# Kernel optimization log

Measured on AMD Instinct MI355X. Metric: run time of the kernel, lower is better.

Reference implementation:

```python
import jax, jax.numpy as jnp
import numpy as np

B, C, Himg, Wimg = 4, 256, 64, 64
HID = 256
K = 8
EPS_NORM = 1e-12
BN_EPS = 1e-5


def setup_inputs() -> dict:
    key = jax.random.key(0)
    ks = jax.random.split(key, 14)
    s = lambda fan: 1.0 / np.sqrt(fan)
    inp = {
        "features": jax.random.normal(ks[0], (B, C, Himg, Wimg), dtype=jnp.float32),
        # HypergraphConv 0: theta (C->HID), phi (HID->HID). Weights stored [in,out].
        "theta0_w": jax.random.normal(ks[1], (C, HID), dtype=jnp.float32) * s(C),
        "theta0_b": jnp.zeros((HID,), jnp.float32),
        "phi0_w": jax.random.normal(ks[2], (HID, HID), dtype=jnp.float32) * s(HID),
        "phi0_b": jnp.zeros((HID,), jnp.float32),
        # HypergraphConv 1: theta (HID->HID), phi (HID->HID)
        "theta1_w": jax.random.normal(ks[3], (HID, HID), dtype=jnp.float32) * s(HID),
        "theta1_b": jnp.zeros((HID,), jnp.float32),
        "phi1_w": jax.random.normal(ks[4], (HID, HID), dtype=jnp.float32) * s(HID),
        "phi1_b": jnp.zeros((HID,), jnp.float32),
        # out_proj: 1x1 conv HID->C, stored as [HID, C]
        "proj_w": jax.random.normal(ks[5], (HID, C), dtype=jnp.float32) * s(HID),
        "proj_b": jnp.zeros((C,), jnp.float32),
        # BatchNorm2d affine params
        "bn_gamma": jnp.ones((C,), jnp.float32),
        "bn_beta": jnp.zeros((C,), jnp.float32),
    }
    return inp


def _build_hypergraph(features):
    # features: [B, C, H, W] -> nodes [B, N, C]; incidence from batch 0 only
    b, c, h, w = features.shape
    n = h * w
    feat_flat = features.reshape(b, c, n).transpose(0, 2, 1)  # [B, N, C]
    f0 = feat_flat[0]  # [N, C] (original computes full-batch similarity but uses [0])
    f0n = f0 / jnp.maximum(jnp.linalg.norm(f0, axis=-1, keepdims=True), EPS_NORM)
    sim = f0n @ f0n.T  # [N, N]
    _, idx = jax.lax.top_k(sim, K)  # [N, K]
    rows = idx.reshape(-1)
    cols = jnp.repeat(jnp.arange(n), K)
    Hm = jnp.zeros((n, n), jnp.float32).at[rows, cols].set(1.0)  # [N, E=N]
    # L1 column normalization (F.normalize p=1 dim=0)
    Hn = Hm / jnp.maximum(Hm.sum(axis=0, keepdims=True), EPS_NORM)
    return Hn, feat_flat


def _hconv(x, Hn, tw, tb, pw, pb):
    # x: [B, N, Cin]
    xt = x @ tw + tb  # [B, N, Cout]
    ef = jnp.einsum('ne,bnc->bec', Hn, xt)  # H^T @ x_theta -> edge feats
    xp = ef @ pw + pb  # [B, E, Cout]
    return jnp.einsum('ne,bec->bnc', Hn, xp)  # H @ x_phi


def reference(features, theta0_w, theta0_b, phi0_w, phi0_b,
              theta1_w, theta1_b, phi1_w, phi1_b,
              proj_w, proj_b, bn_gamma, bn_beta):
    b, c, h, w = features.shape
    Hn, x = _build_hypergraph(features)
    x = jax.nn.relu(_hconv(x, Hn, theta0_w, theta0_b, phi0_w, phi0_b))
    x = jax.nn.relu(_hconv(x, Hn, theta1_w, theta1_b, phi1_w, phi1_b)) + x
    # back to [B, HID, H, W] then 1x1 conv
    x = x.transpose(0, 2, 1).reshape(b, HID, h, w)
    x = jnp.einsum('bihw,io->bohw', x, proj_w) + proj_b[None, :, None, None]
    # BatchNorm2d (training mode: batch statistics, biased variance)
    mean = x.mean(axis=(0, 2, 3))
    var = x.var(axis=(0, 2, 3))
    xn = (x - mean[None, :, None, None]) * jax.lax.rsqrt(var + BN_EPS)[None, :, None, None]
    xn = xn * bn_gamma[None, :, None, None] + bn_beta[None, :, None, None]
    return features + xn
```

## Files before the change

### kernel.cpp

```cpp
#include <hip/hip_runtime.h>

namespace {

constexpr int NB = 4;
constexpr int NC = 256;
constexpr int NN = 4096;

typedef __attribute__((ext_vector_type(8))) short bf8;
typedef __attribute__((ext_vector_type(4))) float f4;
typedef unsigned short ushort_t;
typedef unsigned long long ull;

__device__ __forceinline__ float bf2f(unsigned short u) {
  return __uint_as_float(((unsigned)u) << 16);
}
__device__ __forceinline__ unsigned short f2bf(float f) {
  unsigned x = __float_as_uint(f);
  return (unsigned short)((x + 0x7FFFu + ((x >> 16) & 1u)) >> 16);
}
__device__ __forceinline__ unsigned enc_f(float f) {
  unsigned u = __float_as_uint(f);
  return (u & 0x80000000u) ? ~u : (u | 0x80000000u);
}

__device__ __forceinline__ void insd(double* b, double k) {
  b[7] = fmax(b[7], k);
#pragma unroll
  for (int p = 7; p >= 1; --p) {
    double hi = fmax(b[p-1], b[p]);
    double lo = fmin(b[p-1], b[p]);
    b[p-1] = hi; b[p] = lo;
  }
}

__device__ __forceinline__ double shfl_xor_d(double v, int m) {
  ull u = __double_as_longlong(v);
  unsigned lo = (unsigned)(u & 0xFFFFFFFFull), hi = (unsigned)(u >> 32);
  lo = (unsigned)__shfl_xor((int)lo, m);
  hi = (unsigned)__shfl_xor((int)hi, m);
  return __longlong_as_double(((ull)hi << 32) | (ull)lo);
}

template<int MAXS>
__device__ __forceinline__ void shfl_merged(double* b) {
#pragma unroll
  for (int s = 1; s <= MAXS; s <<= 1) {
    double tmp[8];
#pragma unroll
    for (int k = 0; k < 8; ++k) tmp[k] = shfl_xor_d(b[k], s);
#pragma unroll
    for (int k = 0; k < 8; ++k) insd(b, tmp[k]);
  }
}

__global__ __launch_bounds__(256) void norm_kernel(const float* __restrict__ feat,
                                                   float* __restrict__ inv,
                                                   int* __restrict__ counts,
                                                   float* __restrict__ bnsum) {
  int n = blockIdx.x * 256 + threadIdx.x;
  counts[n] = 0;
  if (n < 2 * NC) bnsum[n] = 0.f;
  float ss = 0.f;
  for (int c = 0; c < NC; ++c) { float v = feat[(size_t)c * NN + n]; ss = fmaf(v, v, ss); }
  inv[n] = 1.f / fmaxf(sqrtf(ss), 1e-12f);
}

__global__ __launch_bounds__(256) void feat2bf_kernel(const float* __restrict__ feat,
                                                      const float* __restrict__ inv,
                                                      unsigned short* __restrict__ xin,
                                                      unsigned short* __restrict__ Xhi,
                                                      unsigned short* __restrict__ Xlo) {
  __shared__ float tile[64][65];
  int n0 = blockIdx.x * 64, c0 = blockIdx.y * 64, b = blockIdx.z;
  int tid = threadIdx.x;
#pragma unroll
  for (int i = 0; i < 4; ++i) {
    int u = tid + i * 256; int cr = u >> 4, q = u & 15;
    float4 v = *(const float4*)&feat[((size_t)b * NC + c0 + cr) * NN + n0 + q * 4];
    tile[cr][q*4+0] = v.x; tile[cr][q*4+1] = v.y; tile[cr][q*4+2] = v.z; tile[cr][q*4+3] = v.w;
  }
  __syncthreads();
#pragma unroll
  for (int i = 0; i < 4; ++i) {
    int u = tid + i * 256; int nr = u >> 4, q = u & 15;
    float x0 = tile[q*4+0][nr], x1 = tile[q*4+1][nr];
    float x2 = tile[q*4+2][nr], x3 = tile[q*4+3][nr];
    ushort4 o;
    o.x = f2bf(x0); o.y = f2bf(x1); o.z = f2bf(x2); o.w = f2bf(x3);
    *(ushort4*)&xin[((size_t)(b << 12) + n0 + nr) * NC + c0 + q * 4] = o;
    if (b == 0) {
      float iv = inv[n0 + nr];
      float y0 = x0 * iv, y1 = x1 * iv, y2 = x2 * iv, y3 = x3 * iv;
      ushort4 h, l;
      h.x = f2bf(y0); l.x = f2bf(y0 - bf2f(h.x));
      h.y = f2bf(y1); l.y = f2bf(y1 - bf2f(h.y));
      h.z = f2bf(y2); l.z = f2bf(y2 - bf2f(h.z));
      h.w = f2bf(y3); l.w = f2bf(y3 - bf2f(h.w));
      size_t oo = (size_t)(n0 + nr) * NC + c0 + q * 4;
      *(ushort4*)&Xhi[oo] = h;
      *(ushort4*)&Xlo[oo] = l;
    }
  }
}

__global__ __launch_bounds__(256) void wcvt_kernel(const float* __restrict__ w0,
                                                   const float* __restrict__ w1,
                                                   const float* __restrict__ w2,
                                                   const float* __restrict__ w3,
                                                   const float* __restrict__ w4,
                                                   unsigned short* __restrict__ Wt) {
  __shared__ float tile[64][65];
  int z = blockIdx.z;
  const float* W = (z == 0) ? w0 : (z == 1) ? w1 : (z == 2) ? w2 : (z == 3) ? w3 : w4;
  int k0 = blockIdx.x * 64, n0 = blockIdx.y * 64;
  int tid = threadIdx.x;
#pragma unroll
  for (int i = 0; i < 4; ++i) {
    int u = tid + i * 256; int kr = u >> 4, q = u & 15;
    float4 v = *(const float4*)&W[(size_t)(k0 + kr) * NC + n0 + q * 4];
    tile[kr][q*4+0] = v.x; tile[kr][q*4+1] = v.y; tile[kr][q*4+2] = v.z; tile[kr][q*4+3] = v.w;
  }
  __syncthreads();
#pragma unroll
  for (int i = 0; i < 4; ++i) {
    int u = tid + i * 256; int nr = u >> 4, q = u & 15;
    ushort4 o;
    o.x = f2bf(tile[q*4+0][nr]); o.y = f2bf(tile[q*4+1][nr]);
    o.z = f2bf(tile[q*4+2][nr]); o.w = f2bf(tile[q*4+3][nr]);
    *(ushort4*)&Wt[(size_t)z * 65536 + (size_t)(n0 + nr) * NC + k0 + q * 4] = o;
  }
}

__global__ __launch_bounds__(512, 6) void simtop_kernel(const unsigned short* __restrict__ Xhi,
                                                        const unsigned short* __restrict__ Xlo,
                                                        double* __restrict__ cand) {
  __shared__ __align__(16) char lds[40960];
  float (*simT)[132] = (float(*)[132])(lds);

  int tid = threadIdx.x, wave = tid >> 6, lane = tid & 63;
  int wm = wave >> 2, wn = wave & 3;
  int orig = blockIdx.x;
  int bid = (orig & 7) * 66 + (orig >> 3);
  int pi = (int)((sqrtf(8.f * (float)bid + 1.f) - 1.f) * 0.5f);
  while ((pi + 1) * (pi + 2) / 2 <= bid) ++pi;
  while (pi * (pi + 1) / 2 > bid) --pi;
  int pj = bid - pi * (pi + 1) / 2;
  int m0 = pj * 128, n0 = pi * 128;

  int sr = tid >> 2;
  int q  = tid & 3;
  int qp = q ^ (sr & 3);
  const ushort_t* gAh = Xhi + (size_t)(m0 + sr) * NC + q * 8;
  const ushort_t* gAl = Xlo + (size_t)(m0 + sr) * NC + q * 8;
  const ushort_t* gBh = Xhi + (size_t)(n0 + sr) * NC + q * 8;
  const ushort_t* gBl = Xlo + (size_t)(n0 + sr) * NC + q * 8;
  int dst = sr * 80 + qp * 16;

  f4 acc[4][2];
#pragma unroll
  for (int i = 0; i < 4; ++i)
#pragma unroll
    for (int j = 0; j < 2; ++j) acc[i][j] = (f4){0.f, 0.f, 0.f, 0.f};

#pragma unroll
  for (int kk = 0; kk < 8; ++kk) {
    uint4 a0 = *(const uint4*)(gAh + kk * 32);
    uint4 a1 = *(const uint4*)(gAl + kk * 32);
    uint4 b0 = *(const uint4*)(gBh + kk * 32);
    uint4 b1 = *(const uint4*)(gBl + kk * 32);
    *(uint4*)(lds +     0 + dst) = a0;
    *(uint4*)(lds + 10240 + dst) = a1;
    *(uint4*)(lds + 20480 + dst) = b0;
    *(uint4*)(lds + 30720 + dst) = b1;
    __syncthreads();
    {
      int qr = lane >> 4;
      bf8 ah[4], al[4], bh[2], bl[2];
#pragma unroll
      for (int mf = 0; mf < 4; ++mf) {
        int rr = wm*64 + mf*16 + (lane & 15);
        int off = rr * 80 + ((qr ^ (rr & 3)) * 16);
        ah[mf] = *(const bf8*)(lds +     0 + off);
        al[mf] = *(const bf8*)(lds + 10240 + off);
      }
#pragma unroll
      for (int nf = 0; nf < 2; ++nf) {
        int rr = wn*32 + nf*16 + (lane & 15);
        int off = rr * 80 + ((qr ^ (rr & 3)) * 16);
        bh[nf] = *(const bf8*)(lds + 20480 + off);
        bl[nf] = *(const bf8*)(lds + 30720 + off);
      }
#pragma unroll
      for (int nf = 0; nf < 2; ++nf)
#pragma unroll
        for (int mf = 0; mf < 4; ++mf) {
          acc[mf][nf] = __builtin_amdgcn_mfma_f32_16x16x32_bf16(ah[mf], bh[nf], acc[mf][nf], 0, 0, 0);
          acc[mf][nf] = __builtin_amdgcn_mfma_f32_16x16x32_bf16(ah[mf], bl[nf], acc[mf][nf], 0, 0, 0);
          acc[mf][nf] = __builtin_amdgcn_mfma_f32_16x16x32_bf16(al[mf], bh[nf], acc[mf][nf], 0, 0, 0);
        }
    }
    __syncthreads();
  }

  double c8[8];
  int ccol = 0, cseg = 0;
  bool docol = (pi != pj) && (tid >= 256);
  if (docol) {
    ccol = (tid - 256) >> 1; cseg = tid & 1;
#pragma unroll
    for (int k = 0; k < 8; ++k) c8[k] = 0.0;
  }

#pragma unroll
  for (int h = 0; h < 2; ++h) {
    if (h) __syncthreads();
    if (wm == h) {
#pragma unroll
      for (int mf = 0; mf < 4; ++mf)
#pragma unroll
        for (int nf = 0; nf < 2; ++nf) {
          int cl = wn*32 + nf*16 + (lane & 15);
          int rb = mf*16 + (lane >> 4)*4;
#pragma unroll
          for (int r = 0; r < 4; ++r) simT[rb + r][cl] = acc[mf][nf][r];
        }
    }
    __syncthreads();
    if (tid < 256) {
      int rl = tid >> 2, q4 = tid & 3;
      const float* rowp = &simT[rl][q4 * 32];
      double b8[8] = {0,0,0,0,0,0,0,0};
#pragma unroll
      for (int i = 0; i < 8; ++i) {
        int off = ((i + q4 * 2) & 7) * 4;
        float4 v = *(const float4*)(rowp + off);
        unsigned jb = 0xFFFu - (unsigned)(n0 + q4 * 32 + off);
        insd(b8, (double)((((ull)enc_f(v.x)) << 12) | (ull)(jb    )));
        insd(b8, (double)((((ull)enc_f(v.y)) << 12) | (ull)(jb - 1)));
        insd(b8, (double)((((ull)enc_f(v.z)) << 12) | (ull)(jb - 2)));
        insd(b8, (double)((((ull)enc_f(v.w)) << 12) | (ull)(jb - 3)));
      }
      shfl_merged<2>(b8);
      if (q4 == 0) {
        double* dp = cand + (size_t)(m0 + h * 64 + rl) * 256 + pi * 8;
#pragma unroll
        for (int k = 0; k < 8; ++k) dp[k] = b8[k];
      }
    } else if (docol) {
#pragma unroll
      for (int i = 0; i < 32; ++i) {
        int ir = (i + cseg * 7) & 31;
        int rloc = cseg * 32 + ir;
        float v = simT[rloc][ccol];
        unsigned jb = 0xFFFu - (unsigned)(m0 + h * 64 + rloc);
        insd(c8, (double)((((ull)enc_f(v)) << 12) | (ull)jb));
      }
    }
  }
  if (docol) {
    shfl_merged<1>(c8);
    if (cseg == 0) {
      double* dp = cand + (size_t)(n0 + ccol) * 256 + pj * 8;
#pragma unroll
      for (int k = 0; k < 8; ++k) dp[k] = c8[k];
    }
  }
}

__global__ __launch_bounds__(256) void merge_kernel(const double* __restrict__ cand,
                                                    int* __restrict__ idx8,
                                                    int* __restrict__ counts) {
  int t = blockIdx.x * 256 + threadIdx.x;
  int row = t >> 3, part = t & 7;
  const double* cp = cand + (size_t)row * 256 + part * 32;
  double b8[8] = {0,0,0,0,0,0,0,0};
  for (int g = 0; g < 4; ++g) {
#pragma unroll 1
    for (int k = 0; k < 8; ++k) {
      double key = cp[g * 8 + k];
      if (key <= b8[7]) break;
      insd(b8, key);
    }
  }
  shfl_merged<4>(b8);
  if (part == 0) {
#pragma unroll
    for (int k = 0; k < 8; ++k) {
      ull K = (ull)b8[k];
      int j = 0xFFF - (int)(K & 0xFFFull);
      idx8[row * 8 + k] = j;
      atomicAdd(&counts[j], 1);
    }
  }
}

__global__ __launch_bounds__(256) void scan_kernel(const int* __restrict__ counts,
                                                   int* __restrict__ offsets,
                                                   int* __restrict__ cursor) {
  __shared__ int ssum[256];
  __shared__ int sbase[257];
  int t = threadIdx.x;
  int loc[16];
  int s = 0;
#pragma unroll
  for (int i = 0; i < 16; ++i) { loc[i] = s; s += counts[t*16 + i]; }
  ssum[t] = s;
  __syncthreads();
  if (t == 0) {
    int acc = 0;
    for (int i = 0; i < 256; ++i) { sbase[i] = acc; acc += ssum[i]; }
    sbase[256] = acc;
  }
  __syncthreads();
  int b0 = sbase[t];
#pragma unroll
  for (int i = 0; i < 16; ++i) {
    int off = b0 + loc[i];
    offsets[t*16 + i] = off;
    cursor [t*16 + i] = off;
  }
  if (t == 0) offsets[NN] = sbase[256];
}

__global__ __launch_bounds__(256) void fill_kernel(const int* __restrict__ idx8,
                                                   int* __restrict__ cursor,
                                                   int* __restrict__ edgelist) {
  int t = blockIdx.x * 256 + threadIdx.x;
  int n = idx8[t];
  int pos = atomicAdd(&cursor[n], 1);
  edgelist[pos] = t >> 3;
}

template<int OUTF32, int BNS, int GATHER>
__global__ __launch_bounds__(512) void gemm_bf16_kernel(const unsigned short* __restrict__ A,
                                                        const unsigned short* __restrict__ Wt,
                                                        const float* __restrict__ bias,
                                                        void* __restrict__ outp,
                                                        float* __restrict__ bnsum,
                                                        const int* __restrict__ idx8) {
  __shared__ ushort_t sA[128][72];
  __shared__ ushort_t sB[128][72];
  __shared__ int sIdx[128][8];
  int tid = threadIdx.x, wave = tid >> 6, lane = tid & 63;
  int wm = wave >> 2, wn = wave & 3;
  int n0 = blockIdx.x * 128, m0 = blockIdx.y * 128;
  size_t bbase = 0;
  if constexpr (GATHER) {
    int e0 = m0 & 4095;
    bbase = ((size_t)(m0 >> 12) << 12) * NC;
#pragma unroll
    for (int u = tid; u < 1024; u += 512) ((int*)sIdx)[u] = idx8[e0 * 8 + u];
    __syncthreads();
  }
  f4 acc[4][2];
#pragma unroll
  for (int i = 0; i < 4; ++i)
#pragma unroll
    for (int j = 0; j < 2; ++j) acc[i][j] = (f4){0.f, 0.f, 0.f, 0.f};

  for (int k0 = 0; k0 < NC; k0 += 64) {
#pragma unroll
    for (int i = 0; i < 2; ++i) {
      int u = tid + i * 512; int r = u >> 3; int qq = u & 7;
      int qp = (qq ^ ((r >> 1) & 7)) * 8;
      if constexpr (GATHER) {
        float s[8] = {0.f,0.f,0.f,0.f,0.f,0.f,0.f,0.f};
#pragma unroll
        for (int k = 0; k < 8; ++k) {
          int nn = sIdx[r][k];
          uint4 v = *(const uint4*)&A[bbase + (size_t)nn * NC + k0 + qq * 8];
          s[0] += bf2f((unsigned short)(v.x & 0xFFFF)); s[1] += bf2f((unsigned short)(v.x >> 16));
          s[2] += bf2f((unsigned short)(v.y & 0xFFFF)); s[3] += bf2f((unsigned short)(v.y >> 16));
          s[4] += bf2f((unsigned short)(v.z & 0xFFFF)); s[5] += bf2f((unsigned short)(v.z >> 16));
          s[6] += bf2f((unsigned short)(v.w & 0xFFFF)); s[7] += bf2f((unsigned short)(v.w >> 16));
        }
        uint4 o;
        o.x = (unsigned)f2bf(s[0]*0.125f) | ((unsigned)f2bf(s[1]*0.125f) << 16);
        o.y = (unsigned)f2bf(s[2]*0.125f) | ((unsigned)f2bf(s[3]*0.125f) << 16);
        o.z = (unsigned)f2bf(s[4]*0.125f) | ((unsigned)f2bf(s[5]*0.125f) << 16);
        o.w = (unsigned)f2bf(s[6]*0.125f) | ((unsigned)f2bf(s[7]*0.125f) << 16);
        *(uint4*)&sA[r][qp] = o;
      } else {
        *(uint4*)&sA[r][qp] = *(const uint4*)&A[(size_t)(m0 + r) * NC + k0 + qq * 8];
      }
      *(uint4*)&sB[r][qp] = *(const uint4*)&Wt[(size_t)(n0 + r) * NC + k0 + qq * 8];
    }
    __syncthreads();
#pragma unroll
    for (int ks = 0; ks < 2; ++ks) {
      int qr = ks * 4 + (lane >> 4);
      bf8 a[4], b[2];
#pragma unroll
      for (int mf = 0; mf < 4; ++mf) {
        int rr = wm*64 + mf*16 + (lane & 15);
        a[mf] = *(const bf8*)&sA[rr][(qr ^ ((rr >> 1) & 7)) * 8];
      }
#pragma unroll
      for (int nf = 0; nf < 2; ++nf) {
        int rr = wn*32 + nf*16 + (lane & 15);
        b[nf] = *(const bf8*)&sB[rr][(qr ^ ((rr >> 1) & 7)) * 8];
      }
#pragma unroll
      for (int nf = 0; nf < 2; ++nf)
#pragma unroll
        for (int mf = 0; mf < 4; ++mf)
          acc[mf][nf] = __builtin_amdgcn_mfma_f32_16x16x32_bf16(a[mf], b[nf], acc[mf][nf], 0, 0, 0);
    }
    __syncthreads();
  }
#pragma unroll
  for (int nf = 0; nf < 2; ++nf) {
    int n = n0 + wn*32 + nf*16 + (lane & 15);
    float bi = bias[n];
    float s1 = 0.f, s2 = 0.f;
#pragma unroll
    for (int mf = 0; mf < 4; ++mf) {
#pragma unroll
      for (int r = 0; r < 4; ++r) {
        int m = m0 + wm*64 + mf*16 + (lane >> 4)*4 + r;
        float v = acc[mf][nf][r] + bi;
        if (OUTF32) ((float*)outp)[(size_t)m * NC + n] = v;
        else ((unsigned short*)outp)[(size_t)m * NC + n] = f2bf(v);
        if (BNS) { s1 += v; s2 = fmaf(v, v, s2); }
      }
    }
    if (BNS) {
      s1 += __shfl_xor(s1, 16); s1 += __shfl_xor(s1, 32);
      s2 += __shfl_xor(s2, 16); s2 += __shfl_xor(s2, 32);
      if (lane < 16) {
        atomicAdd(&bnsum[n], s1);
        atomicAdd(&bnsum[NC + n], s2);
      }
    }
  }
}

template<int MODE>
__global__ __launch_bounds__(256) void scatter_kernel(const unsigned short* __restrict__ xp,
                                                      const int* __restrict__ offsets,
                                                      const int* __restrict__ edgelist,
                                                      const unsigned short* __restrict__ res,
                                                      unsigned short* __restrict__ outb) {
  int b = blockIdx.y;
  int n = blockIdx.x * 4 + (threadIdx.x >> 6);
  int lane = threadIdx.x & 63;
  int s0i = offsets[n], s1i = offsets[n + 1];
  float s0 = 0, s1 = 0, s2 = 0, s3 = 0;
  for (int j = s0i; j < s1i; ++j) {
    int e = edgelist[j];
    uint2 v = *(const uint2*)&xp[((size_t)((b << 12) + e)) * NC + lane * 4];
    s0 += bf2f((unsigned short)(v.x & 0xFFFF)); s1 += bf2f((unsigned short)(v.x >> 16));
    s2 += bf2f((unsigned short)(v.y & 0xFFFF)); s3 += bf2f((unsigned short)(v.y >> 16));
  }
  s0 = fmaxf(s0 * 0.125f, 0.f); s1 = fmaxf(s1 * 0.125f, 0.f);
  s2 = fmaxf(s2 * 0.125f, 0.f); s3 = fmaxf(s3 * 0.125f, 0.f);
  size_t o = ((size_t)((b << 12) + n)) * NC + lane * 4;
  if (MODE == 1) {
    uint2 v = *(const uint2*)&res[o];
    s0 += bf2f((unsigned short)(v.x & 0xFFFF)); s1 += bf2f((unsigned short)(v.x >> 16));
    s2 += bf2f((unsigned short)(v.y & 0xFFFF)); s3 += bf2f((unsigned short)(v.y >> 16));
  }
  uint2 ov;
  ov.x = (unsigned)f2bf(s0) | ((unsigned)f2bf(s1) << 16);
  ov.y = (unsigned)f2bf(s2) | ((unsigned)f2bf(s3) << 16);
  *(uint2*)&outb[o] = ov;
}

__global__ __launch_bounds__(256) void final_kernel(const float* __restrict__ y,
                                                    const float* __restrict__ feat,
                                                    const float* __restrict__ bnsum,
                                                    const float* __restrict__ gam,
                                                    const float* __restrict__ bet,
                                                    float* __restrict__ out) {
  __shared__ float tile[64][65];
  __shared__ float sa_[64], sb_[64];
  int n0 = blockIdx.x * 64;
  int c0 = blockIdx.y * 64;
  int b  = blockIdx.z;
  int tid = threadIdx.x;
  if (tid < 64) {
    const float invn = 1.f / (float)(NB * NN);
    int c = c0 + tid;
    float mean = bnsum[c] * invn;
    float var  = bnsum[NC + c] * invn - mean * mean;
    float a = gam[c] * rsqrtf(var + 1e-5f);
    sa_[tid] = a;
    sb_[tid] = bet[c] - mean * a;
  }
  int n_l = tid >> 2;
  int q   = tid & 3;
  const float4* y4 = (const float4*)y;
#pragma unroll
  for (int i = 0; i < 4; ++i) {
    int cl = q * 16 + i * 4;
    float4 v = y4[(size_t)(b * NN + n0 + n_l) * 64 + ((c0 + cl) >> 2)];
    tile[n_l][cl+0] = v.x; tile[n_l][cl+1] = v.y; tile[n_l][cl+2] = v.z; tile[n_l][cl+3] = v.w;
  }
  __syncthreads();
  int cl2 = tid >> 6;
  int nl2 = tid & 63;
#pragma unroll
  for (int p = 0; p < 16; ++p) {
    int ci = p * 4 + cl2;
    float a = sa_[ci], bb = sb_[ci];
    size_t o = (size_t)b * (NC * NN) + (size_t)(c0 + ci) * NN + n0 + nl2;
    out[o] = feat[o] + fmaf(a, tile[nl2][ci], bb);
  }
}

}

extern "C" void kernel_launch(void* const* d_in, const int* in_sizes, int n_in,
                              void* d_out, int out_size, void* d_ws, size_t ws_size,
                              hipStream_t stream) {
  (void)in_sizes; (void)n_in; (void)out_size; (void)ws_size;
  const float* feat = (const float*)d_in[0];
  const float* t0w  = (const float*)d_in[1];
  const float* t0b  = (const float*)d_in[2];
  const float* p0w  = (const float*)d_in[3];
  const float* p0b  = (const float*)d_in[4];
  const float* t1w  = (const float*)d_in[5];
  const float* t1b  = (const float*)d_in[6];
  const float* p1w  = (const float*)d_in[7];
  const float* p1b  = (const float*)d_in[8];
  const float* pw   = (const float*)d_in[9];
  const float* pb   = (const float*)d_in[10];
  const float* gam  = (const float*)d_in[11];
  const float* bet  = (const float*)d_in[12];
  float* out = (float*)d_out;

  char* ws = (char*)d_ws;
  float*          y   = (float*)ws;
  unsigned short* xin = (unsigned short*)(ws + (16u << 20));
  unsigned short* xt  = (unsigned short*)(ws + (24u << 20));
  unsigned short* xp  = (unsigned short*)(ws + (40u << 20));
  unsigned short* x1  = (unsigned short*)(ws + (48u << 20));
  unsigned short* x2  = (unsigned short*)(ws + (56u << 20));
  unsigned short* Xhi = (unsigned short*)(ws + (64u << 20));
  unsigned short* Xlo = (unsigned short*)(ws + (66u << 20));
  double*         cand = (double*)(ws + (68u << 20));
  char* sm = ws + (76u << 20);
  unsigned short* Wt  = (unsigned short*)sm;
  int*   idx8     = (int*)(sm + 655360);
  int*   counts   = (int*)(sm + 786432);
  int*   offsets  = (int*)(sm + 802816);
  int*   cursor   = (int*)(sm + 819456);
  int*   edgelist = (int*)(sm + 835840);
  float* inv      = (float*)(sm + 966912);
  float* bnsum    = (float*)(sm + 983296);

  norm_kernel<<<NN / 256, 256, 0, stream>>>(feat, inv, counts, bnsum);
  feat2bf_kernel<<<dim3(64, 4, 4), 256, 0, stream>>>(feat, inv, xin, Xhi, Xlo);
  wcvt_kernel<<<dim3(4, 4, 5), 256, 0, stream>>>(t0w, p0w, t1w, p1w, pw, Wt);

  simtop_kernel<<<528, 512, 0, stream>>>(Xhi, Xlo, cand);
  merge_kernel<<<128, 256, 0, stream>>>(cand, idx8, counts);
  scan_kernel<<<1, 256, 0, stream>>>(counts, offsets, cursor);
  fill_kernel<<<128, 256, 0, stream>>>(idx8, cursor, edgelist);

  gemm_bf16_kernel<0,0,0><<<dim3(2, 128), 512, 0, stream>>>(xin, Wt + 0*65536, t0b, xt, nullptr, nullptr);
  gemm_bf16_kernel<0,0,1><<<dim3(2, 128), 512, 0, stream>>>(xt,  Wt + 1*65536, p0b, xp, nullptr, idx8);
  scatter_kernel<0><<<dim3(1024, 4), 256, 0, stream>>>(xp, offsets, edgelist, nullptr, x1);
  gemm_bf16_kernel<0,0,0><<<dim3(2, 128), 512, 0, stream>>>(x1, Wt + 2*65536, t1b, xt, nullptr, nullptr);
  gemm_bf16_kernel<0,0,1><<<dim3(2, 128), 512, 0, stream>>>(xt, Wt + 3*65536, p1b, xp, nullptr, idx8);
  scatter_kernel<1><<<dim3(1024, 4), 256, 0, stream>>>(xp, offsets, edgelist, x1, x2);
  gemm_bf16_kernel<1,1,0><<<dim3(2, 128), 512, 0, stream>>>(x2, Wt + 4*65536, pb, y, bnsum, nullptr);

  final_kernel<<<dim3(64, 4, 4), 256, 0, stream>>>(y, feat, bnsum, gam, bet, out);
}
```

Measured before the change: 307.7 us.

## Fold theta and phi weights into one matrix per hypergraph conv

Since the edge aggregation H^T is linear and columns of Hn sum to one, theta followed by phi is algebraically merged: W' = theta_w @ phi_w and b' = theta_b @ phi_w + phi_b are precomputed once per call by small GEMMs and a bias kernel. Each conv layer then runs a single gathered GEMM on the input instead of a theta GEMM plus a gathered phi GEMM, removing two full-size GEMM launches and the xt intermediate traffic. The cost is extra rounding from quantizing the combined weight to bf16, and the bias folding relies on every edge column having nonzero degree, which holds for top-k incidence.

```diff
diff --git a/kernel.cpp b/kernel.cpp
--- a/kernel.cpp
+++ b/kernel.cpp
@@ -103,17 +103,28 @@
   }
 }
 
-__global__ __launch_bounds__(256) void wcvt_kernel(const float* __restrict__ w0,
-                                                   const float* __restrict__ w1,
-                                                   const float* __restrict__ w2,
-                                                   const float* __restrict__ w3,
-                                                   const float* __restrict__ w4,
+__global__ __launch_bounds__(256) void wcvt_kernel(const float* __restrict__ p0w,
+                                                   const float* __restrict__ p1w,
+                                                   const float* __restrict__ pw,
+                                                   const float* __restrict__ t0w,
+                                                   const float* __restrict__ t1w,
                                                    unsigned short* __restrict__ Wt) {
   __shared__ float tile[64][65];
   int z = blockIdx.z;
-  const float* W = (z == 0) ? w0 : (z == 1) ? w1 : (z == 2) ? w2 : (z == 3) ? w3 : w4;
+  const float* W = (z == 0) ? p0w : (z == 1) ? p1w : (z == 2) ? pw : (z == 3) ? t0w : t1w;
   int k0 = blockIdx.x * 64, n0 = blockIdx.y * 64;
   int tid = threadIdx.x;
+  if (z >= 3) {
+#pragma unroll
+    for (int i = 0; i < 4; ++i) {
+      int u = tid + i * 256; int kr = u >> 4, q = u & 15;
+      float4 v = *(const float4*)&W[(size_t)(k0 + kr) * NC + n0 + q * 4];
+      ushort4 o;
+      o.x = f2bf(v.x); o.y = f2bf(v.y); o.z = f2bf(v.z); o.w = f2bf(v.w);
+      *(ushort4*)&Wt[(size_t)z * 65536 + (size_t)(k0 + kr) * NC + n0 + q * 4] = o;
+    }
+    return;
+  }
 #pragma unroll
   for (int i = 0; i < 4; ++i) {
     int u = tid + i * 256; int kr = u >> 4, q = u & 15;
@@ -129,6 +140,22 @@
     o.z = f2bf(tile[q*4+2][nr]); o.w = f2bf(tile[q*4+3][nr]);
     *(ushort4*)&Wt[(size_t)z * 65536 + (size_t)(n0 + nr) * NC + k0 + q * 4] = o;
   }
+}
+
+__global__ __launch_bounds__(256) void bprime_kernel(const float* __restrict__ tb0,
+                                                     const float* __restrict__ pw0,
+                                                     const float* __restrict__ pb0,
+                                                     const float* __restrict__ tb1,
+                                                     const float* __restrict__ pw1,
+                                                     const float* __restrict__ pb1,
+                                                     float* __restrict__ bp) {
+  int z = blockIdx.x, n = threadIdx.x;
+  const float* tb = z ? tb1 : tb0;
+  const float* pw = z ? pw1 : pw0;
+  const float* pb = z ? pb1 : pb0;
+  float s = pb[n];
+  for (int k = 0; k < NC; ++k) s = fmaf(tb[k], pw[(size_t)k * NC + n], s);
+  bp[z * NC + n] = s;
 }
 
 __global__ __launch_bounds__(512, 6) void simtop_kernel(const unsigned short* __restrict__ Xhi,
@@ -331,7 +358,7 @@
   edgelist[pos] = t >> 3;
 }
 
-template<int OUTF32, int BNS, int GATHER>
+template<int OUTMODE, int BNS, int GATHER>
 __global__ __launch_bounds__(512) void gemm_bf16_kernel(const unsigned short* __restrict__ A,
                                                         const unsigned short* __restrict__ Wt,
                                                         const float* __restrict__ bias,
@@ -411,7 +438,8 @@
 #pragma unroll
   for (int nf = 0; nf < 2; ++nf) {
     int n = n0 + wn*32 + nf*16 + (lane & 15);
-    float bi = bias[n];
+    float bi = 0.f;
+    if constexpr (OUTMODE != 2) bi = bias[n];
     float s1 = 0.f, s2 = 0.f;
 #pragma unroll
     for (int mf = 0; mf < 4; ++mf) {
@@ -419,12 +447,13 @@
       for (int r = 0; r < 4; ++r) {
         int m = m0 + wm*64 + mf*16 + (lane >> 4)*4 + r;
         float v = acc[mf][nf][r] + bi;
-        if (OUTF32) ((float*)outp)[(size_t)m * NC + n] = v;
+        if constexpr (OUTMODE == 1) ((float*)outp)[(size_t)m * NC + n] = v;
+        else if constexpr (OUTMODE == 2) ((unsigned short*)outp)[(size_t)n * NC + m] = f2bf(v);
         else ((unsigned short*)outp)[(size_t)m * NC + n] = f2bf(v);
-        if (BNS) { s1 += v; s2 = fmaf(v, v, s2); }
-      }
-    }
-    if (BNS) {
+        if constexpr (BNS) { s1 += v; s2 = fmaf(v, v, s2); }
+      }
+    }
+    if constexpr (BNS) {
       s1 += __shfl_xor(s1, 16); s1 += __shfl_xor(s1, 32);
       s2 += __shfl_xor(s2, 16); s2 += __shfl_xor(s2, 32);
       if (lane < 16) {
@@ -532,7 +561,6 @@
   char* ws = (char*)d_ws;
   float*          y   = (float*)ws;
   unsigned short* xin = (unsigned short*)(ws + (16u << 20));
-  unsigned short* xt  = (unsigned short*)(ws + (24u << 20));
   unsigned short* xp  = (unsigned short*)(ws + (40u << 20));
   unsigned short* x1  = (unsigned short*)(ws + (48u << 20));
   unsigned short* x2  = (unsigned short*)(ws + (56u << 20));
@@ -541,30 +569,34 @@
   double*         cand = (double*)(ws + (68u << 20));
   char* sm = ws + (76u << 20);
   unsigned short* Wt  = (unsigned short*)sm;
-  int*   idx8     = (int*)(sm + 655360);
-  int*   counts   = (int*)(sm + 786432);
-  int*   offsets  = (int*)(sm + 802816);
-  int*   cursor   = (int*)(sm + 819456);
-  int*   edgelist = (int*)(sm + 835840);
-  float* inv      = (float*)(sm + 966912);
-  float* bnsum    = (float*)(sm + 983296);
+  int*   idx8     = (int*)(sm + 917504);
+  int*   counts   = (int*)(sm + 1048576);
+  int*   offsets  = (int*)(sm + 1064960);
+  int*   cursor   = (int*)(sm + 1081472);
+  int*   edgelist = (int*)(sm + 1097856);
+  float* inv      = (float*)(sm + 1228928);
+  float* bnsum    = (float*)(sm + 1245312);
+  float* bp       = (float*)(sm + 1247360);
 
   norm_kernel<<<NN / 256, 256, 0, stream>>>(feat, inv, counts, bnsum);
   feat2bf_kernel<<<dim3(64, 4, 4), 256, 0, stream>>>(feat, inv, xin, Xhi, Xlo);
-  wcvt_kernel<<<dim3(4, 4, 5), 256, 0, stream>>>(t0w, p0w, t1w, p1w, pw, Wt);
+  wcvt_kernel<<<dim3(4, 4, 5), 256, 0, stream>>>(p0w, p1w, pw, t0w, t1w, Wt);
+  gemm_bf16_kernel<2,0,0><<<dim3(2, 2), 512, 0, stream>>>(Wt + 3*65536, Wt + 0*65536, nullptr,
+                                                          Wt + 5*65536, nullptr, nullptr);
+  gemm_bf16_kernel<2,0,0><<<dim3(2, 2), 512, 0, stream>>>(Wt + 4*65536, Wt + 1*65536, nullptr,
+                                                          Wt + 6*65536, nullptr, nullptr);
+  bprime_kernel<<<2, 256, 0, stream>>>(t0b, p0w, p0b, t1b, p1w, p1b, bp);
 
   simtop_kernel<<<528, 512, 0, stream>>>(Xhi, Xlo, cand);
   merge_kernel<<<128, 256, 0, stream>>>(cand, idx8, counts);
   scan_kernel<<<1, 256, 0, stream>>>(counts, offsets, cursor);
   fill_kernel<<<128, 256, 0, stream>>>(idx8, cursor, edgelist);
 
-  gemm_bf16_kernel<0,0,0><<<dim3(2, 128), 512, 0, stream>>>(xin, Wt + 0*65536, t0b, xt, nullptr, nullptr);
-  gemm_bf16_kernel<0,0,1><<<dim3(2, 128), 512, 0, stream>>>(xt,  Wt + 1*65536, p0b, xp, nullptr, idx8);
+  gemm_bf16_kernel<0,0,1><<<dim3(2, 128), 512, 0, stream>>>(xin, Wt + 5*65536, bp, xp, nullptr, idx8);
   scatter_kernel<0><<<dim3(1024, 4), 256, 0, stream>>>(xp, offsets, edgelist, nullptr, x1);
-  gemm_bf16_kernel<0,0,0><<<dim3(2, 128), 512, 0, stream>>>(x1, Wt + 2*65536, t1b, xt, nullptr, nullptr);
-  gemm_bf16_kernel<0,0,1><<<dim3(2, 128), 512, 0, stream>>>(xt, Wt + 3*65536, p1b, xp, nullptr, idx8);
+  gemm_bf16_kernel<0,0,1><<<dim3(2, 128), 512, 0, stream>>>(x1, Wt + 6*65536, bp + NC, xp, nullptr, idx8);
   scatter_kernel<1><<<dim3(1024, 4), 256, 0, stream>>>(xp, offsets, edgelist, x1, x2);
-  gemm_bf16_kernel<1,1,0><<<dim3(2, 128), 512, 0, stream>>>(x2, Wt + 4*65536, pb, y, bnsum, nullptr);
+  gemm_bf16_kernel<1,1,0><<<dim3(2, 128), 512, 0, stream>>>(x2, Wt + 2*65536, pb, y, bnsum, nullptr);
 
   final_kernel<<<dim3(64, 4, 4), 256, 0, stream>>>(y, feat, bnsum, gam, bet, out);
 }
```

Measured after the change: 315.9 us. +2.7%, slower.
